# Performance work log

Hardware: AMD Instinct MI355X
Metric: run time of the kernel (lower is better)

## Reference

```python
import jax, jax.numpy as jnp
import numpy as np

NUM_USERS = 100000
NUM_ITEMS = 50000
D = 64            # args.recdim
N_LAYERS = 3      # args.layer
NNZ = 4800000     # edges in the normalized bipartite adjacency (COO)
N = NUM_USERS + NUM_ITEMS


def setup_inputs() -> dict:
    key = jax.random.key(0)
    k1, k2, k3, k4, k5 = jax.random.split(key, 5)
    # LightGCN inits embeddings with normal(std=0.1)
    user_emb = 0.1 * jax.random.normal(k1, (NUM_USERS, D), dtype=jnp.float32)
    item_emb = 0.1 * jax.random.normal(k2, (NUM_ITEMS, D), dtype=jnp.float32)
    adj_rows = jax.random.randint(k3, (NNZ,), 0, N)
    adj_cols = jax.random.randint(k4, (NNZ,), 0, N)
    # stand-in for D^{-1/2} A D^{-1/2} normalized values
    adj_vals = jax.random.uniform(k5, (NNZ,), dtype=jnp.float32)
    return {"user_emb": user_emb, "item_emb": item_emb,
            "adj_vals": adj_vals, "adj_rows": adj_rows, "adj_cols": adj_cols}


def _spmm(rows, cols, vals, x, n):
    # sparse [n,n] @ dense [n,d] via gather + segment-sum (COO SpMM)
    return jax.ops.segment_sum(vals[:, None] * x[cols], rows, num_segments=n)


def reference(user_emb, item_emb, adj_vals, adj_rows, adj_cols):
    n_users = user_emb.shape[0]
    n = n_users + item_emb.shape[0]
    all_emb = jnp.concatenate([user_emb, item_emb], axis=0)  # [N, D]
    embs = [all_emb]
    for _ in range(N_LAYERS):  # fixed small hop count
        all_emb = _spmm(adj_rows, adj_cols, adj_vals, all_emb, n)
        embs.append(all_emb)
    light_out = jnp.mean(jnp.stack(embs, axis=1), axis=1)  # [N, D]
    users = light_out[:n_users]
    items = light_out[n_users:]
    return users, items
```

## Files before the change

kernel.cpp:

```cpp
#include <hip/hip_runtime.h>


#define NUSERS 100000
#define NITEMS 50000
#define NTOT   150000
#define DIM    64
#define NNZ_E  4800000

#define RPB     256
#define RSH     8
#define NBUCK   586
#define CHUNK_E 8192
#define NPART   ((NNZ_E + CHUNK_E - 1) / CHUNK_E)
#define NCB     74
#define CSH     11
#define NBIN    (64 * NCB)
#define NOCT    (NBUCK * 64)

__device__ __forceinline__ unsigned short benc(float f) {
    union { float f; unsigned u; } t; t.f = f;
    unsigned r = t.u + 0x7FFFu + ((t.u >> 16) & 1u);
    return (unsigned short)(r >> 16);
}
__device__ __forceinline__ float blo(unsigned g) { return __uint_as_float(g << 16); }
__device__ __forceinline__ float bhi(unsigned g) { return __uint_as_float(g & 0xFFFF0000u); }

__global__ void __launch_bounds__(512)
partA1_kernel(const int* __restrict__ rows, int* __restrict__ cntmat) {
    __shared__ int l[NBUCK];
    int p = blockIdx.x;
    int c0 = p * CHUNK_E;
    int c1 = c0 + CHUNK_E; if (c1 > NNZ_E) c1 = NNZ_E;
    for (int k = threadIdx.x; k < NBUCK; k += 512) l[k] = 0;
    __syncthreads();
    for (int e = c0 + threadIdx.x; e < c1; e += 512)
        atomicAdd(&l[rows[e] >> RSH], 1);
    __syncthreads();
    for (int k = threadIdx.x; k < NBUCK; k += 512)
        cntmat[(size_t)p * NBUCK + k] = l[k];
}

__global__ void __launch_bounds__(1024)
colscan1_kernel(const int* __restrict__ cntmat, int* __restrict__ runoffT,
                int* __restrict__ colTotal) {
    __shared__ int t[1024];
    int b = blockIdx.x;
    int tid = threadIdx.x;
    int v = (tid < NPART) ? cntmat[(size_t)tid * NBUCK + b] : 0;
    t[tid] = v;
    __syncthreads();
    for (int ofs = 1; ofs < 1024; ofs <<= 1) {
        int a = (tid >= ofs) ? t[tid - ofs] : 0;
        __syncthreads();
        t[tid] += a;
        __syncthreads();
    }
    if (tid < NPART) runoffT[(size_t)b * (NPART + 1) + tid] = t[tid] - v;
    if (tid == NPART - 1) {
        runoffT[(size_t)b * (NPART + 1) + NPART] = t[tid];
        colTotal[b] = t[tid];
    }
}

__global__ void __launch_bounds__(1024)
colscan2_kernel(const int* __restrict__ colTotal, int* __restrict__ bptr) {
    __shared__ int t[1024];
    int tid = threadIdx.x;
    int v = (tid < NBUCK) ? colTotal[tid] : 0;
    t[tid] = v;
    __syncthreads();
    for (int ofs = 1; ofs < 1024; ofs <<= 1) {
        int a = (tid >= ofs) ? t[tid - ofs] : 0;
        __syncthreads();
        t[tid] += a;
        __syncthreads();
    }
    if (tid < NBUCK) bptr[tid] = t[tid] - v;
    if (tid == 1023) bptr[NBUCK] = t[1023];
}

__global__ void __launch_bounds__(512)
partA2_kernel(const int* __restrict__ rows, const int* __restrict__ cols,
              const float* __restrict__ vals, const int* __restrict__ cntmat,
              int* __restrict__ segoff, int2* __restrict__ tmp) {
    __shared__ int2 buf[CHUNK_E];
    __shared__ int cur[NBUCK];
    __shared__ int st[512];
    int p = blockIdx.x;
    int c0 = p * CHUNK_E;
    int c1 = c0 + CHUNK_E; if (c1 > NNZ_E) c1 = NNZ_E;
    int nb = c1 - c0;
    int tid = threadIdx.x;
    int t0 = tid * 2;
    int cA = (t0     < NBUCK) ? cntmat[(size_t)p * NBUCK + t0]     : 0;
    int cB = (t0 + 1 < NBUCK) ? cntmat[(size_t)p * NBUCK + t0 + 1] : 0;
    int s = cA + cB;
    st[tid] = s;
    __syncthreads();
    for (int ofs = 1; ofs < 512; ofs <<= 1) {
        int a = (tid >= ofs) ? st[tid - ofs] : 0;
        __syncthreads();
        st[tid] += a;
        __syncthreads();
    }
    int P = st[tid] - s;
    if (t0     < NBUCK) { cur[t0]     = P;      segoff[(size_t)p * NBUCK + t0]     = P; }
    if (t0 + 1 < NBUCK) { cur[t0 + 1] = P + cA; segoff[(size_t)p * NBUCK + t0 + 1] = P + cA; }
    __syncthreads();
    for (int e = c0 + tid; e < c1; e += 512) {
        int r = rows[e];
        int b = r >> RSH, rl = r & (RPB - 1);
        int q = atomicAdd(&cur[b], 1);
        buf[q] = make_int2(cols[e] | (rl << 18), __float_as_int(vals[e]));
    }
    __syncthreads();
    for (int k = tid; k < nb; k += 512)
        tmp[c0 + k] = buf[k];
}

__global__ void __launch_bounds__(1024)
partBF_kernel(const int* __restrict__ bptr, const int* __restrict__ runoffT,
              const int* __restrict__ segoff, const int2* __restrict__ tmp,
              unsigned* __restrict__ fin, int* __restrict__ optr) {
    __shared__ int cnt[NBIN];
    __shared__ int base[NBIN];
    __shared__ int st[1024];
    __shared__ int runoff[NPART + 1];
    __shared__ int soff[NPART];
    int b = blockIdx.x;
    int bb0 = bptr[b];
    int tid = threadIdx.x;
    for (int k = tid; k < NBIN; k += 1024) cnt[k] = 0;
    if (tid <= NPART) runoff[tid] = runoffT[(size_t)b * (NPART + 1) + tid];
    if (tid < NPART)  soff[tid]   = segoff[(size_t)tid * NBUCK + b];
    __syncthreads();
    int nb = runoff[NPART];
    for (int j = tid; j < nb; j += 1024) {
        int lo = 0, hi = NPART;
        while (hi - lo > 1) { int mid = (lo + hi) >> 1; if (runoff[mid] <= j) lo = mid; else hi = mid; }
        int src = lo * CHUNK_E + soff[lo] + (j - runoff[lo]);
        int x = tmp[src].x;
        int key = ((x >> 20) & 63) * NCB + ((x & 0x3FFFF) >> CSH);
        atomicAdd(&cnt[key], 1);
    }
    __syncthreads();
    int t0 = tid * 5;
    int c0 = (t0     < NBIN) ? cnt[t0]     : 0;
    int c1 = (t0 + 1 < NBIN) ? cnt[t0 + 1] : 0;
    int c2 = (t0 + 2 < NBIN) ? cnt[t0 + 2] : 0;
    int c3 = (t0 + 3 < NBIN) ? cnt[t0 + 3] : 0;
    int c4 = (t0 + 4 < NBIN) ? cnt[t0 + 4] : 0;
    int s = c0 + c1 + c2 + c3 + c4;
    st[tid] = s;
    __syncthreads();
    for (int ofs = 1; ofs < 1024; ofs <<= 1) {
        int a = (tid >= ofs) ? st[tid - ofs] : 0;
        __syncthreads();
        st[tid] += a;
        __syncthreads();
    }
    int P = st[tid] - s;
    if (t0     < NBIN) base[t0]     = P;
    if (t0 + 1 < NBIN) base[t0 + 1] = P + c0;
    if (t0 + 2 < NBIN) base[t0 + 2] = P + c0 + c1;
    if (t0 + 3 < NBIN) base[t0 + 3] = P + c0 + c1 + c2;
    if (t0 + 4 < NBIN) base[t0 + 4] = P + c0 + c1 + c2 + c3;
    __syncthreads();
    if (tid < 64) optr[b * 64 + tid] = bb0 + base[tid * NCB];
    if (b == NBUCK - 1 && tid == 0) optr[NBUCK * 64] = bb0 + nb;
    __syncthreads();
    for (int j = tid; j < nb; j += 1024) {
        int lo = 0, hi = NPART;
        while (hi - lo > 1) { int mid = (lo + hi) >> 1; if (runoff[mid] <= j) lo = mid; else hi = mid; }
        int src = lo * CHUNK_E + soff[lo] + (j - runoff[lo]);
        int2 t = tmp[src];
        int x = t.x;
        int key = ((x >> 20) & 63) * NCB + ((x & 0x3FFFF) >> CSH);
        int q = atomicAdd(&base[key], 1);
        unsigned qq = (unsigned)__float2int_rn(__int_as_float(t.y) * 4096.f);
        if (qq > 4095u) qq = 4095u;
        fin[bb0 + q] = ((unsigned)x & 0xFFFFFu) | (qq << 20);
    }
}

__global__ void convert_kernel(const float2* __restrict__ user, const float2* __restrict__ item,
                               unsigned* __restrict__ xh2) {
    int i = blockIdx.x * blockDim.x + threadIdx.x;
    if (i >= NTOT * 32) return;
    float2 v = (i < NUSERS * 32) ? user[i] : item[i - NUSERS * 32];
    xh2[i] = (unsigned)benc(v.x) | ((unsigned)benc(v.y) << 16);
}

__global__ void __launch_bounds__(256)
spmm4_kernel(const int* __restrict__ optr, const unsigned* __restrict__ ed,
             const uint4* __restrict__ xin, uint4* __restrict__ yout,
             const float4* __restrict__ user, const float4* __restrict__ item,
             const uint4* __restrict__ y1, float4* __restrict__ out, int last) {
    int wid  = blockIdx.x * 4 + (threadIdx.x >> 6);
    int lane = threadIdx.x & 63;
    int g    = wid * 8 + (lane >> 3);
    int s    = lane & 7;
    int i    = optr[g];
    int end  = optr[g + 1];
    const float SCL = 1.f / 4096.f;
    float4 A00 = {0,0,0,0}, A01 = {0,0,0,0};
    float4 A10 = {0,0,0,0}, A11 = {0,0,0,0};
    float4 A20 = {0,0,0,0}, A21 = {0,0,0,0};
    float4 A30 = {0,0,0,0}, A31 = {0,0,0,0};

#define PROC(E, G) do { \
        float v  = (float)((E) >> 20) * SCL; \
        int   k  = ((E) >> 18) & 3; \
        float s0 = (k == 0) ? v : 0.f, s1 = (k == 1) ? v : 0.f; \
        float s2 = (k == 2) ? v : 0.f, s3 = (k == 3) ? v : 0.f; \
        float f0 = blo((G).x), f1 = bhi((G).x), f2 = blo((G).y), f3 = bhi((G).y); \
        float f4_ = blo((G).z), f5 = bhi((G).z), f6 = blo((G).w), f7 = bhi((G).w); \
        A00.x += s0*f0; A00.y += s0*f1; A00.z += s0*f2; A00.w += s0*f3; \
        A01.x += s0*f4_; A01.y += s0*f5; A01.z += s0*f6; A01.w += s0*f7; \
        A10.x += s1*f0; A10.y += s1*f1; A10.z += s1*f2; A10.w += s1*f3; \
        A11.x += s1*f4_; A11.y += s1*f5; A11.z += s1*f6; A11.w += s1*f7; \
        A20.x += s2*f0; A20.y += s2*f1; A20.z += s2*f2; A20.w += s2*f3; \
        A21.x += s2*f4_; A21.y += s2*f5; A21.z += s2*f6; A21.w += s2*f7; \
        A30.x += s3*f0; A30.y += s3*f1; A30.z += s3*f2; A30.w += s3*f3; \
        A31.x += s3*f4_; A31.y += s3*f5; A31.z += s3*f6; A31.w += s3*f7; \
    } while (0)

    for (; i + 4 <= end; i += 4) {
        unsigned e0 = ed[i], e1 = ed[i + 1], e2 = ed[i + 2], e3 = ed[i + 3];
        uint4 g0 = xin[(size_t)(e0 & 0x3FFFF) * 8 + s];
        uint4 g1 = xin[(size_t)(e1 & 0x3FFFF) * 8 + s];
        uint4 g2 = xin[(size_t)(e2 & 0x3FFFF) * 8 + s];
        uint4 g3 = xin[(size_t)(e3 & 0x3FFFF) * 8 + s];
        PROC(e0, g0); PROC(e1, g1); PROC(e2, g2); PROC(e3, g3);
    }
    for (; i < end; ++i) {
        unsigned e = ed[i];
        uint4 gg = xin[(size_t)(e & 0x3FFFF) * 8 + s];
        PROC(e, gg);
    }
#undef PROC

    if (!last) {
#define EPI(K, AK0, AK1) do { \
        int r = g * 4 + (K); \
        if (r < NTOT) { \
            uint4 o; \
            o.x = (unsigned)benc(AK0.x) | ((unsigned)benc(AK0.y) << 16); \
            o.y = (unsigned)benc(AK0.z) | ((unsigned)benc(AK0.w) << 16); \
            o.z = (unsigned)benc(AK1.x) | ((unsigned)benc(AK1.y) << 16); \
            o.w = (unsigned)benc(AK1.z) | ((unsigned)benc(AK1.w) << 16); \
            yout[(size_t)r * 8 + s] = o; \
        } \
    } while (0)
        EPI(0, A00, A01); EPI(1, A10, A11); EPI(2, A20, A21); EPI(3, A30, A31);
#undef EPI
    } else {
#define EPI(K, AK0, AK1) do { \
        int r = g * 4 + (K); \
        if (r < NTOT) { \
            size_t f4 = (size_t)r * 16 + 2 * s; \
            float4 x0a = (r < NUSERS) ? user[f4]     : item[f4     - (size_t)NUSERS * 16]; \
            float4 x0b = (r < NUSERS) ? user[f4 + 1] : item[f4 + 1 - (size_t)NUSERS * 16]; \
            uint4 u1 = y1[(size_t)r * 8 + s]; \
            uint4 u2 = xin[(size_t)r * 8 + s]; \
            float4 oa, ob; \
            oa.x = 0.25f * (x0a.x + blo(u1.x) + blo(u2.x) + AK0.x); \
            oa.y = 0.25f * (x0a.y + bhi(u1.x) + bhi(u2.x) + AK0.y); \
            oa.z = 0.25f * (x0a.z + blo(u1.y) + blo(u2.y) + AK0.z); \
            oa.w = 0.25f * (x0a.w + bhi(u1.y) + bhi(u2.y) + AK0.w); \
            ob.x = 0.25f * (x0b.x + blo(u1.z) + blo(u2.z) + AK1.x); \
            ob.y = 0.25f * (x0b.y + bhi(u1.z) + bhi(u2.z) + AK1.y); \
            ob.z = 0.25f * (x0b.z + blo(u1.w) + blo(u2.w) + AK1.z); \
            ob.w = 0.25f * (x0b.w + bhi(u1.w) + bhi(u2.w) + AK1.w); \
            out[f4]     = oa; \
            out[f4 + 1] = ob; \
        } \
    } while (0)
        EPI(0, A00, A01); EPI(1, A10, A11); EPI(2, A20, A21); EPI(3, A30, A31);
#undef EPI
    }
}

extern "C" void kernel_launch(void* const* d_in, const int* in_sizes, int n_in,
                              void* d_out, int out_size, void* d_ws, size_t ws_size,
                              hipStream_t stream) {
    const float* user = (const float*)d_in[0];
    const float* item = (const float*)d_in[1];
    const float* vals = (const float*)d_in[2];
    const int*   rows = (const int*)d_in[3];
    const int*   cols = (const int*)d_in[4];
    float* out = (float*)d_out;

    char* w = (char*)d_ws;
    int2*     tmp      = (int2*)w;     w += (size_t)NNZ_E * 8;
    unsigned* fin      = (unsigned*)w; w += (size_t)NNZ_E * 4;
    unsigned* bufA     = (unsigned*)w; w += (size_t)NTOT * DIM * 2;
    unsigned* bufB     = (unsigned*)w; w += (size_t)NTOT * DIM * 2;
    int*      cntmat   = (int*)w;      w += (size_t)NPART * NBUCK * 4;
    int*      runoffT  = (int*)w;      w += (size_t)NBUCK * (NPART + 1) * 4;
    int*      segoff   = (int*)w;      w += (size_t)NPART * NBUCK * 4;
    int*      optr     = (int*)w;      w += (size_t)(NOCT + 1) * 4;
    int*      colTotal = (int*)w;      w += (size_t)NBUCK * 4;
    int*      bptr     = (int*)w;

    const int blk = 256;
    const int gConv = (NTOT * 32 + blk - 1) / blk;
    const int gSpmm = NOCT / 32;

    partA1_kernel<<<NPART, 512, 0, stream>>>(rows, cntmat);
    colscan1_kernel<<<NBUCK, 1024, 0, stream>>>(cntmat, runoffT, colTotal);
    colscan2_kernel<<<1, 1024, 0, stream>>>(colTotal, bptr);
    partA2_kernel<<<NPART, 512, 0, stream>>>(rows, cols, vals, cntmat, segoff, tmp);
    partBF_kernel<<<NBUCK, 1024, 0, stream>>>(bptr, runoffT, segoff, tmp, fin, optr);

    convert_kernel<<<gConv, blk, 0, stream>>>((const float2*)user, (const float2*)item, bufA);

    spmm4_kernel<<<gSpmm, blk, 0, stream>>>(optr, fin, (const uint4*)bufA, (uint4*)bufB,
                                            (const float4*)user, (const float4*)item,
                                            (const uint4*)bufB, (float4*)out, 0);
    spmm4_kernel<<<gSpmm, blk, 0, stream>>>(optr, fin, (const uint4*)bufB, (uint4*)bufA,
                                            (const float4*)user, (const float4*)item,
                                            (const uint4*)bufB, (float4*)out, 0);
    spmm4_kernel<<<gSpmm, blk, 0, stream>>>(optr, fin, (const uint4*)bufA, (uint4*)bufA,
                                            (const float4*)user, (const float4*)item,
                                            (const uint4*)bufB, (float4*)out, 1);
}
```

Before: 475.0 us.

## Fuse edge counting into partition scatter and read bf16 layer-0 in epilogue

Merges the per-chunk bucket histogram kernel into the scatter kernel: each thread keeps its 16 row indices in registers, counts with shared atomics, scans locally, then scatters, removing one full pass over the row array and a kernel launch. The final layer epilogue now reads the bf16 converted layer-0 embeddings instead of the fp32 user/item arrays, halving that read, and intermediate buffers alias the temporary edge workspace to shrink footprint. Using bf16 for the layer-0 term slightly reduces accuracy of the output mean.

```diff
diff --git a/kernel.cpp b/kernel.cpp
--- a/kernel.cpp
+++ b/kernel.cpp
@@ -26,18 +26,64 @@
 __device__ __forceinline__ float bhi(unsigned g) { return __uint_as_float(g & 0xFFFF0000u); }
 
 __global__ void __launch_bounds__(512)
-partA1_kernel(const int* __restrict__ rows, int* __restrict__ cntmat) {
-    __shared__ int l[NBUCK];
+partA2_kernel(const int* __restrict__ rows, const int* __restrict__ cols,
+              const float* __restrict__ vals, int* __restrict__ cntmat,
+              int* __restrict__ segoff, int2* __restrict__ tmp) {
+    __shared__ int2 buf[CHUNK_E];
+    __shared__ int cnt[NBUCK];
+    __shared__ int st[512];
     int p = blockIdx.x;
     int c0 = p * CHUNK_E;
     int c1 = c0 + CHUNK_E; if (c1 > NNZ_E) c1 = NNZ_E;
-    for (int k = threadIdx.x; k < NBUCK; k += 512) l[k] = 0;
-    __syncthreads();
-    for (int e = c0 + threadIdx.x; e < c1; e += 512)
-        atomicAdd(&l[rows[e] >> RSH], 1);
-    __syncthreads();
-    for (int k = threadIdx.x; k < NBUCK; k += 512)
-        cntmat[(size_t)p * NBUCK + k] = l[k];
+    int nb = c1 - c0;
+    int tid = threadIdx.x;
+    for (int k = tid; k < NBUCK; k += 512) cnt[k] = 0;
+    __syncthreads();
+    int rloc[16];
+#pragma unroll
+    for (int u = 0; u < 16; ++u) {
+        int e = c0 + tid + u * 512;
+        rloc[u] = (e < c1) ? rows[e] : -1;
+        if (rloc[u] >= 0) atomicAdd(&cnt[rloc[u] >> RSH], 1);
+    }
+    __syncthreads();
+    int t0 = tid * 2;
+    int cA = (t0     < NBUCK) ? cnt[t0]     : 0;
+    int cB = (t0 + 1 < NBUCK) ? cnt[t0 + 1] : 0;
+    int s = cA + cB;
+    st[tid] = s;
+    __syncthreads();
+    for (int ofs = 1; ofs < 512; ofs <<= 1) {
+        int a = (tid >= ofs) ? st[tid - ofs] : 0;
+        __syncthreads();
+        st[tid] += a;
+        __syncthreads();
+    }
+    int P = st[tid] - s;
+    if (t0 < NBUCK) {
+        cnt[t0] = P;
+        segoff[(size_t)p * NBUCK + t0] = P;
+        cntmat[(size_t)p * NBUCK + t0] = cA;
+    }
+    if (t0 + 1 < NBUCK) {
+        cnt[t0 + 1] = P + cA;
+        segoff[(size_t)p * NBUCK + t0 + 1] = P + cA;
+        cntmat[(size_t)p * NBUCK + t0 + 1] = cB;
+    }
+    __syncthreads();
+#pragma unroll
+    for (int u = 0; u < 16; ++u) {
+        int e = c0 + tid + u * 512;
+        if (rloc[u] >= 0) {
+            int r = rloc[u];
+            int b = r >> RSH, rl = r & (RPB - 1);
+            int q = atomicAdd(&cnt[b], 1);
+            buf[q] = make_int2(cols[e] | (rl << 18), __float_as_int(vals[e]));
+        }
+    }
+    __syncthreads();
+    for (int k = tid; k < nb; k += 512)
+        tmp[c0 + k] = buf[k];
 }
 
 __global__ void __launch_bounds__(1024)
@@ -77,45 +123,6 @@
     }
     if (tid < NBUCK) bptr[tid] = t[tid] - v;
     if (tid == 1023) bptr[NBUCK] = t[1023];
-}
-
-__global__ void __launch_bounds__(512)
-partA2_kernel(const int* __restrict__ rows, const int* __restrict__ cols,
-              const float* __restrict__ vals, const int* __restrict__ cntmat,
-              int* __restrict__ segoff, int2* __restrict__ tmp) {
-    __shared__ int2 buf[CHUNK_E];
-    __shared__ int cur[NBUCK];
-    __shared__ int st[512];
-    int p = blockIdx.x;
-    int c0 = p * CHUNK_E;
-    int c1 = c0 + CHUNK_E; if (c1 > NNZ_E) c1 = NNZ_E;
-    int nb = c1 - c0;
-    int tid = threadIdx.x;
-    int t0 = tid * 2;
-    int cA = (t0     < NBUCK) ? cntmat[(size_t)p * NBUCK + t0]     : 0;
-    int cB = (t0 + 1 < NBUCK) ? cntmat[(size_t)p * NBUCK + t0 + 1] : 0;
-    int s = cA + cB;
-    st[tid] = s;
-    __syncthreads();
-    for (int ofs = 1; ofs < 512; ofs <<= 1) {
-        int a = (tid >= ofs) ? st[tid - ofs] : 0;
-        __syncthreads();
-        st[tid] += a;
-        __syncthreads();
-    }
-    int P = st[tid] - s;
-    if (t0     < NBUCK) { cur[t0]     = P;      segoff[(size_t)p * NBUCK + t0]     = P; }
-    if (t0 + 1 < NBUCK) { cur[t0 + 1] = P + cA; segoff[(size_t)p * NBUCK + t0 + 1] = P + cA; }
-    __syncthreads();
-    for (int e = c0 + tid; e < c1; e += 512) {
-        int r = rows[e];
-        int b = r >> RSH, rl = r & (RPB - 1);
-        int q = atomicAdd(&cur[b], 1);
-        buf[q] = make_int2(cols[e] | (rl << 18), __float_as_int(vals[e]));
-    }
-    __syncthreads();
-    for (int k = tid; k < nb; k += 512)
-        tmp[c0 + k] = buf[k];
 }
 
 __global__ void __launch_bounds__(1024)
@@ -194,8 +201,8 @@
 __global__ void __launch_bounds__(256)
 spmm4_kernel(const int* __restrict__ optr, const unsigned* __restrict__ ed,
              const uint4* __restrict__ xin, uint4* __restrict__ yout,
-             const float4* __restrict__ user, const float4* __restrict__ item,
-             const uint4* __restrict__ y1, float4* __restrict__ out, int last) {
+             const uint4* __restrict__ x0h, const uint4* __restrict__ y1,
+             float4* __restrict__ out, int last) {
     int wid  = blockIdx.x * 4 + (threadIdx.x >> 6);
     int lane = threadIdx.x & 63;
     int g    = wid * 8 + (lane >> 3);
@@ -258,20 +265,19 @@
 #define EPI(K, AK0, AK1) do { \
         int r = g * 4 + (K); \
         if (r < NTOT) { \
-            size_t f4 = (size_t)r * 16 + 2 * s; \
-            float4 x0a = (r < NUSERS) ? user[f4]     : item[f4     - (size_t)NUSERS * 16]; \
-            float4 x0b = (r < NUSERS) ? user[f4 + 1] : item[f4 + 1 - (size_t)NUSERS * 16]; \
+            uint4 u0 = x0h[(size_t)r * 8 + s]; \
             uint4 u1 = y1[(size_t)r * 8 + s]; \
             uint4 u2 = xin[(size_t)r * 8 + s]; \
+            size_t f4 = (size_t)r * 16 + 2 * s; \
             float4 oa, ob; \
-            oa.x = 0.25f * (x0a.x + blo(u1.x) + blo(u2.x) + AK0.x); \
-            oa.y = 0.25f * (x0a.y + bhi(u1.x) + bhi(u2.x) + AK0.y); \
-            oa.z = 0.25f * (x0a.z + blo(u1.y) + blo(u2.y) + AK0.z); \
-            oa.w = 0.25f * (x0a.w + bhi(u1.y) + bhi(u2.y) + AK0.w); \
-            ob.x = 0.25f * (x0b.x + blo(u1.z) + blo(u2.z) + AK1.x); \
-            ob.y = 0.25f * (x0b.y + bhi(u1.z) + bhi(u2.z) + AK1.y); \
-            ob.z = 0.25f * (x0b.z + blo(u1.w) + blo(u2.w) + AK1.z); \
-            ob.w = 0.25f * (x0b.w + bhi(u1.w) + bhi(u2.w) + AK1.w); \
+            oa.x = 0.25f * (blo(u0.x) + blo(u1.x) + blo(u2.x) + AK0.x); \
+            oa.y = 0.25f * (bhi(u0.x) + bhi(u1.x) + bhi(u2.x) + AK0.y); \
+            oa.z = 0.25f * (blo(u0.y) + blo(u1.y) + blo(u2.y) + AK0.z); \
+            oa.w = 0.25f * (bhi(u0.y) + bhi(u1.y) + bhi(u2.y) + AK0.w); \
+            ob.x = 0.25f * (blo(u0.z) + blo(u1.z) + blo(u2.z) + AK1.x); \
+            ob.y = 0.25f * (bhi(u0.z) + bhi(u1.z) + bhi(u2.z) + AK1.y); \
+            ob.z = 0.25f * (blo(u0.w) + blo(u1.w) + blo(u2.w) + AK1.z); \
+            ob.w = 0.25f * (bhi(u0.w) + bhi(u1.w) + bhi(u2.w) + AK1.w); \
             out[f4]     = oa; \
             out[f4 + 1] = ob; \
         } \
@@ -292,10 +298,9 @@
     float* out = (float*)d_out;
 
     char* w = (char*)d_ws;
-    int2*     tmp      = (int2*)w;     w += (size_t)NNZ_E * 8;
+    char*     X        = w;            w += (size_t)NNZ_E * 8;
     unsigned* fin      = (unsigned*)w; w += (size_t)NNZ_E * 4;
-    unsigned* bufA     = (unsigned*)w; w += (size_t)NTOT * DIM * 2;
-    unsigned* bufB     = (unsigned*)w; w += (size_t)NTOT * DIM * 2;
+    unsigned* bufX     = (unsigned*)w; w += (size_t)NTOT * DIM * 2;
     int*      cntmat   = (int*)w;      w += (size_t)NPART * NBUCK * 4;
     int*      runoffT  = (int*)w;      w += (size_t)NBUCK * (NPART + 1) * 4;
     int*      segoff   = (int*)w;      w += (size_t)NPART * NBUCK * 4;
@@ -303,25 +308,28 @@
     int*      colTotal = (int*)w;      w += (size_t)NBUCK * 4;
     int*      bptr     = (int*)w;
 
+    int2*     tmp  = (int2*)X;
+    unsigned* bufB = (unsigned*)X;
+    unsigned* bufC = (unsigned*)(X + (size_t)NTOT * DIM * 2);
+
     const int blk = 256;
     const int gConv = (NTOT * 32 + blk - 1) / blk;
     const int gSpmm = NOCT / 32;
 
-    partA1_kernel<<<NPART, 512, 0, stream>>>(rows, cntmat);
+    partA2_kernel<<<NPART, 512, 0, stream>>>(rows, cols, vals, cntmat, segoff, tmp);
     colscan1_kernel<<<NBUCK, 1024, 0, stream>>>(cntmat, runoffT, colTotal);
     colscan2_kernel<<<1, 1024, 0, stream>>>(colTotal, bptr);
-    partA2_kernel<<<NPART, 512, 0, stream>>>(rows, cols, vals, cntmat, segoff, tmp);
     partBF_kernel<<<NBUCK, 1024, 0, stream>>>(bptr, runoffT, segoff, tmp, fin, optr);
 
-    convert_kernel<<<gConv, blk, 0, stream>>>((const float2*)user, (const float2*)item, bufA);
-
-    spmm4_kernel<<<gSpmm, blk, 0, stream>>>(optr, fin, (const uint4*)bufA, (uint4*)bufB,
-                                            (const float4*)user, (const float4*)item,
-                                            (const uint4*)bufB, (float4*)out, 0);
-    spmm4_kernel<<<gSpmm, blk, 0, stream>>>(optr, fin, (const uint4*)bufB, (uint4*)bufA,
-                                            (const float4*)user, (const float4*)item,
-                                            (const uint4*)bufB, (float4*)out, 0);
-    spmm4_kernel<<<gSpmm, blk, 0, stream>>>(optr, fin, (const uint4*)bufA, (uint4*)bufA,
-                                            (const float4*)user, (const float4*)item,
-                                            (const uint4*)bufB, (float4*)out, 1);
-}
+    convert_kernel<<<gConv, blk, 0, stream>>>((const float2*)user, (const float2*)item, bufX);
+
+    spmm4_kernel<<<gSpmm, blk, 0, stream>>>(optr, fin, (const uint4*)bufX, (uint4*)bufB,
+                                            (const uint4*)bufX, (const uint4*)bufB,
+                                            (float4*)out, 0);
+    spmm4_kernel<<<gSpmm, blk, 0, stream>>>(optr, fin, (const uint4*)bufB, (uint4*)bufC,
+                                            (const uint4*)bufX, (const uint4*)bufB,
+                                            (float4*)out, 0);
+    spmm4_kernel<<<gSpmm, blk, 0, stream>>>(optr, fin, (const uint4*)bufC, (uint4*)bufC,
+                                            (const uint4*)bufX, (const uint4*)bufB,
+                                            (float4*)out, 1);
+}
```

New measurement: 466.4 us. Within noise of the previous version (-1.8%).
